# Kernel optimization log

Measured on AMD Instinct MI355X. Metric: run time of the kernel, lower is better.

## Reference

```python
import jax, jax.numpy as jnp
import numpy as np

EMBED_DIM = 1024
NUM_HEADS = 16
HEAD_DIM = EMBED_DIM // NUM_HEADS
B, S = 2, 2048


def setup_inputs() -> dict:
    key = jax.random.key(0)
    ks = jax.random.split(key, 11)
    scale = 1.0 / np.sqrt(EMBED_DIM)
    inp = {
        "q": jax.random.normal(ks[0], (B, S, EMBED_DIM), jnp.float32),
        "k": jax.random.normal(ks[1], (B, S, EMBED_DIM), jnp.float32),
        "v": jax.random.normal(ks[2], (B, S, EMBED_DIM), jnp.float32),
        "Wq": jax.random.normal(ks[3], (EMBED_DIM, EMBED_DIM), jnp.float32) * scale,
        "bq": jnp.zeros((EMBED_DIM,), jnp.float32),
        "Wk": jax.random.normal(ks[4], (EMBED_DIM, EMBED_DIM), jnp.float32) * scale,
        "bk": jnp.zeros((EMBED_DIM,), jnp.float32),
        "Wv": jax.random.normal(ks[5], (EMBED_DIM, EMBED_DIM), jnp.float32) * scale,
        "bv": jnp.zeros((EMBED_DIM,), jnp.float32),
        "Wo": jax.random.normal(ks[6], (EMBED_DIM, EMBED_DIM), jnp.float32) * scale,
        "bo": jnp.zeros((EMBED_DIM,), jnp.float32),
    }
    return inp


def _split_heads(x):
    # [B, S, E] -> [B, H, S, D]
    b, s, _ = x.shape
    return x.reshape(b, s, NUM_HEADS, HEAD_DIM).transpose(0, 2, 1, 3)


def reference(q, k, v, Wq, bq, Wk, bk, Wv, bv, Wo, bo):
    query = _split_heads(q @ Wq + bq)  # [B,H,S,D]
    key_ = _split_heads(k @ Wk + bk)
    value = _split_heads(v @ Wv + bv)
    # scaled dot-product attention (scale by sqrt(head_dim), as in source)
    logits = jnp.einsum("bhqd,bhkd->bhqk", query, key_) / jnp.sqrt(
        jnp.asarray(HEAD_DIM, jnp.float32)
    )
    weights = jax.nn.softmax(logits, axis=-1)
    attn = jnp.einsum("bhqk,bhkd->bhqd", weights, value)  # [B,H,S,D]
    concat = attn.transpose(0, 2, 1, 3).reshape(q.shape[0], -1, EMBED_DIM)
    return concat @ Wo + bo
```

## Files before the change

### kernel.cpp

```cpp
#include <hip/hip_runtime.h>
#include <hip/hip_bf16.h>
#include <math.h>


typedef short bf16x8 __attribute__((ext_vector_type(8)));
typedef short bf16x4 __attribute__((ext_vector_type(4)));
typedef float f32x4 __attribute__((ext_vector_type(4)));
typedef unsigned short u16;
typedef unsigned int u32;

#if defined(__HIP_DEVICE_COMPILE__) && __has_builtin(__builtin_amdgcn_mfma_f32_16x16x16_bf16)
#define MFMA16(a, b, c) __builtin_amdgcn_mfma_f32_16x16x16_bf16(a, b, c, 0, 0, 0)
#else
#define MFMA16(a, b, c) __builtin_amdgcn_mfma_f32_16x16x16bf16_1k(a, b, c, 0, 0, 0)
#endif

#define QSCALE 0.18033688011112042f

__device__ __forceinline__ u16 f2b(float f) {
  union { float f; unsigned u; } v; v.f = f;
  unsigned r = v.u + 0x7FFF + ((v.u >> 16) & 1);
  return (u16)(r >> 16);
}

__device__ __forceinline__ void glds16(const u16* g, u16* l) {
  __builtin_amdgcn_global_load_lds(
      (const __attribute__((address_space(1))) u32*)g,
      (__attribute__((address_space(3))) u32*)l, 16, 0, 0);
}

__global__ void prep(const float* __restrict__ q, const float* __restrict__ k,
                     const float* __restrict__ v, u16* __restrict__ qo,
                     u16* __restrict__ ko, u16* __restrict__ vo,
                     const float* __restrict__ W0, const float* __restrict__ W1,
                     const float* __restrict__ W2, const float* __restrict__ W3,
                     u16* __restrict__ T0, u16* __restrict__ T1,
                     u16* __restrict__ T2, u16* __restrict__ T3) {
  const int z = blockIdx.y;
  if (z < 3) {
    const float* in = z == 0 ? q : (z == 1 ? k : v);
    u16* out = z == 0 ? qo : (z == 1 ? ko : vo);
    int i = (blockIdx.x * 256 + threadIdx.x) * 8;
    float4 a = *(const float4*)(in + i);
    float4 b = *(const float4*)(in + i + 4);
    union { u16 u[8]; uint4 v; } o;
    o.u[0] = f2b(a.x); o.u[1] = f2b(a.y); o.u[2] = f2b(a.z); o.u[3] = f2b(a.w);
    o.u[4] = f2b(b.x); o.u[5] = f2b(b.y); o.u[6] = f2b(b.z); o.u[7] = f2b(b.w);
    *(uint4*)(out + i) = o.v;
    return;
  }
  if (blockIdx.x >= 256) return;
  const int zz = z - 3;
  const float* W = zz == 0 ? W0 : (zz == 1 ? W1 : (zz == 2 ? W2 : W3));
  u16* WT = zz == 0 ? T0 : (zz == 1 ? T1 : (zz == 2 ? T2 : T3));
  __shared__ float tile[64][65];
  int k0 = (blockIdx.x >> 4) * 64, n0 = (blockIdx.x & 15) * 64;
  int c = threadIdx.x & 63, r0 = threadIdx.x >> 6;
  #pragma unroll
  for (int i = 0; i < 64; i += 4)
    tile[r0 + i][c] = W[(k0 + r0 + i) * 1024 + n0 + c];
  __syncthreads();
  #pragma unroll
  for (int i = 0; i < 64; i += 4)
    WT[(n0 + r0 + i) * 1024 + k0 + c] = f2b(tile[c][r0 + i]);
}

template<int MODE, int BN>
__device__ __forceinline__ void gemm_core(
    const u16* __restrict__ A, const u16* __restrict__ BT,
    const float* __restrict__ bias, void* __restrict__ out,
    int bx, int by, float scale) {
  constexpr int NT = BN / 64 * 2;
  __shared__ u16 As[128 * 64];
  __shared__ u16 Bs[BN * 64];
  const int tid = threadIdx.x;
  const int w = tid >> 6, lane = tid & 63;
  const int wm = w >> 1, wn = w & 1;
  const int q = lane >> 4, l16 = lane & 15;
  const int m0 = by * 128, n0 = bx * BN;
  const int K = 1024;

  f32x4 acc[4][NT] = {};
  for (int k0 = 0; k0 < K; k0 += 64) {
    __syncthreads();
    #pragma unroll
    for (int p = 0; p < 4; ++p) {
      int c = p * 4 + w;
      int ci = c * 64 + lane;
      int r = ci >> 3, b = ci & 7;
      glds16(A + (m0 + r) * K + k0 + ((b ^ (r & 7)) * 8), As + c * 512);
    }
    #pragma unroll
    for (int p = 0; p < BN / 32; ++p) {
      int c = p * 4 + w;
      int ci = c * 64 + lane;
      int r = ci >> 3, b = ci & 7;
      glds16(BT + (n0 + r) * K + k0 + ((b ^ (r & 7)) * 8), Bs + c * 512);
    }
    __builtin_amdgcn_s_waitcnt(0xF70);
    __syncthreads();
    #pragma unroll
    for (int ks = 0; ks < 2; ++ks) {
      bf16x8 af[4], bf[NT];
      #pragma unroll
      for (int mt = 0; mt < 4; ++mt) {
        int row = wm * 64 + mt * 16 + l16;
        af[mt] = *(const bf16x8*)(As + row * 64 + (((ks * 4 + q) ^ (row & 7)) * 8));
      }
      #pragma unroll
      for (int nt = 0; nt < NT; ++nt) {
        int row = wn * (BN / 2) + nt * 16 + l16;
        bf[nt] = *(const bf16x8*)(Bs + row * 64 + (((ks * 4 + q) ^ (row & 7)) * 8));
      }
      #pragma unroll
      for (int mt = 0; mt < 4; ++mt)
        #pragma unroll
        for (int nt = 0; nt < NT; ++nt)
          acc[mt][nt] = __builtin_amdgcn_mfma_f32_16x16x32_bf16(af[mt], bf[nt], acc[mt][nt], 0, 0, 0);
    }
  }
  #pragma unroll
  for (int mt = 0; mt < 4; ++mt)
    #pragma unroll
    for (int nt = 0; nt < NT; ++nt) {
      int col = n0 + wn * (BN / 2) + nt * 16 + l16;
      float bcol = bias[col];
      if (MODE == 2) {
        int rbase = m0 + wm * 64 + mt * 16 + q * 4;
        int b = rbase >> 11, s0 = rbase & 2047;
        int h = col >> 6, d = col & 63;
        union { u16 u[4]; uint2 v; } o;
        #pragma unroll
        for (int reg = 0; reg < 4; ++reg)
          o.u[reg] = f2b(acc[mt][nt][reg] + bcol);
        *(uint2*)((u16*)out + (((b << 4) + h) * 64 + d) * 2048 + s0) = o.v;
      } else {
        #pragma unroll
        for (int reg = 0; reg < 4; ++reg) {
          int row = m0 + wm * 64 + mt * 16 + q * 4 + reg;
          float val = (acc[mt][nt][reg] + bcol) * scale;
          if (MODE == 0) {
            int b = row >> 11, s = row & 2047, h = col >> 6, d = col & 63;
            ((u16*)out)[(((b << 4) + h) * 2048 + s) * 64 + d] = f2b(val);
          } else {
            ((float*)out)[row * 1024 + col] = val;
          }
        }
      }
    }
}

__global__ __launch_bounds__(256) void gemm_qkv(
    const u16* qb, const u16* kb, const u16* vb,
    const u16* WqT, const u16* WkT, const u16* WvT,
    const float* bq, const float* bk, const float* bv,
    u16* Qh, u16* Kh, u16* VhT) {
  int z = blockIdx.z;
  if (z == 0)      gemm_core<0, 128>(qb, WqT, bq, Qh,  blockIdx.x, blockIdx.y, QSCALE);
  else if (z == 1) gemm_core<0, 128>(kb, WkT, bk, Kh,  blockIdx.x, blockIdx.y, 1.0f);
  else             gemm_core<2, 128>(vb, WvT, bv, VhT, blockIdx.x, blockIdx.y, 1.0f);
}

__global__ __launch_bounds__(256) void gemm_out(
    const u16* A, const u16* BT, const float* bias, float* out) {
  gemm_core<1, 64>(A, BT, bias, out, blockIdx.x, blockIdx.y, 1.0f);
}

__global__ __launch_bounds__(256) void flash_attn(
    const u16* __restrict__ Qh, const u16* __restrict__ Kh,
    const u16* __restrict__ VTh, u16* __restrict__ Oo) {
  __shared__ u16 Ks[2][4096];
  __shared__ u16 Vt[2][4096];

  const int tid = threadIdx.x, w = tid >> 6, lane = tid & 63;
  const int q = lane >> 4, l16 = lane & 15;
  const int bh = blockIdx.x & 31, qt = blockIdx.x >> 5;
  const u16* Qp = Qh + (bh * 2048 + qt * 128) * 64;
  const u16* Kp = Kh + bh * 2048 * 64;
  const u16* Vp = VTh + bh * 64 * 2048;

  bf16x8 aq[2][2];
  #pragma unroll
  for (int rb = 0; rb < 2; ++rb)
    #pragma unroll
    for (int ks = 0; ks < 2; ++ks)
      aq[rb][ks] = *(const bf16x8*)(Qp + (w * 32 + rb * 16 + l16) * 64 + ks * 32 + q * 8);

  const int sr = (lane & 7) ^ (lane >> 3);
  auto stage = [&](int kt2, int buf) {
    #pragma unroll
    for (int p = 0; p < 2; ++p) {
      int c = p * 4 + w;
      int r = c * 8 + (lane >> 3);
      glds16(Kp + (kt2 * 64 + r) * 64 + sr * 8, &Ks[buf][c * 512]);
      glds16(Vp + r * 2048 + kt2 * 64 + sr * 8, &Vt[buf][c * 512]);
    }
  };
  stage(0, 0);

  f32x4 oacc[4][2] = {};
  float lacc[2] = {0.f, 0.f};

  for (int kt = 0; kt < 32; ++kt) {
    const int buf = kt & 1;
    __builtin_amdgcn_s_waitcnt(0xF70);
    __syncthreads();
    if (kt + 1 < 32) stage(kt + 1, buf ^ 1);

    const u16* KsT = Ks[buf];
    const u16* VtT = Vt[buf];

    f32x4 st[2][4] = {};
    #pragma unroll
    for (int ks = 0; ks < 2; ++ks) {
      bf16x8 bk[4];
      #pragma unroll
      for (int nt = 0; nt < 4; ++nt) {
        int row = nt * 16 + l16;
        bk[nt] = *(const bf16x8*)(KsT + row * 64 + (((ks * 4 + q) ^ (l16 & 7)) * 8));
      }
      #pragma unroll
      for (int rb = 0; rb < 2; ++rb)
        #pragma unroll
        for (int nt = 0; nt < 4; ++nt)
          st[rb][nt] = __builtin_amdgcn_mfma_f32_16x16x32_bf16(bk[nt], aq[rb][ks], st[rb][nt], 0, 0, 0);
    }

    #pragma unroll
    for (int rb = 0; rb < 2; ++rb)
      #pragma unroll
      for (int nt = 0; nt < 4; ++nt)
        #pragma unroll
        for (int reg = 0; reg < 4; ++reg) {
          float p = __builtin_amdgcn_exp2f(st[rb][nt][reg]);
          lacc[rb] += p;
          st[rb][nt][reg] = p;
        }

    #pragma unroll
    for (int kb = 0; kb < 4; ++kb) {
      bf16x4 pf[2];
      #pragma unroll
      for (int rb = 0; rb < 2; ++rb) {
        union { u32 u[2]; bf16x4 v; } pk;
        pk.u[0] = __builtin_amdgcn_perm(__float_as_uint(st[rb][kb][1]),
                                        __float_as_uint(st[rb][kb][0]), 0x07060302u);
        pk.u[1] = __builtin_amdgcn_perm(__float_as_uint(st[rb][kb][3]),
                                        __float_as_uint(st[rb][kb][2]), 0x07060302u);
        pf[rb] = pk.v;
      }
      #pragma unroll
      for (int ntd = 0; ntd < 4; ++ntd) {
        int row = ntd * 16 + l16;
        int c = kb * 2 + (q >> 1);
        bf16x4 vf = *(const bf16x4*)(VtT + row * 64 + ((c ^ (l16 & 7)) * 8) + (q & 1) * 4);
        #pragma unroll
        for (int rb = 0; rb < 2; ++rb)
          oacc[ntd][rb] = MFMA16(vf, pf[rb], oacc[ntd][rb]);
      }
    }
  }

  float rl[2];
  #pragma unroll
  for (int rb = 0; rb < 2; ++rb) {
    float s = lacc[rb];
    s += __shfl_xor(s, 16);
    s += __shfl_xor(s, 32);
    rl[rb] = 0.998046875f / s;
  }

  const int b = bh >> 4, h = bh & 15;
  #pragma unroll
  for (int rb = 0; rb < 2; ++rb) {
    int row = b * 2048 + qt * 128 + w * 32 + rb * 16 + l16;
    #pragma unroll
    for (int ntd = 0; ntd < 4; ++ntd) {
      union { u16 u[4]; uint2 v; } o;
      #pragma unroll
      for (int reg = 0; reg < 4; ++reg)
        o.u[reg] = f2b(oacc[ntd][rb][reg] * rl[rb]);
      *(uint2*)(Oo + row * 1024 + h * 64 + ntd * 16 + q * 4) = o.v;
    }
  }
}

extern "C" void kernel_launch(void* const* d_in, const int* in_sizes, int n_in,
                              void* d_out, int out_size, void* d_ws, size_t ws_size,
                              hipStream_t stream) {
  const float* q  = (const float*)d_in[0];
  const float* k  = (const float*)d_in[1];
  const float* v  = (const float*)d_in[2];
  const float* Wq = (const float*)d_in[3];
  const float* bq = (const float*)d_in[4];
  const float* Wk = (const float*)d_in[5];
  const float* bk = (const float*)d_in[6];
  const float* Wv = (const float*)d_in[7];
  const float* bv = (const float*)d_in[8];
  const float* Wo = (const float*)d_in[9];
  const float* bo = (const float*)d_in[10];

  char* ws = (char*)d_ws;
  const size_t MB = 1024 * 1024;
  u16* qb  = (u16*)(ws);
  u16* kb  = (u16*)(ws + 8 * MB);
  u16* vb  = (u16*)(ws + 16 * MB);
  u16* WqT = (u16*)(ws + 24 * MB);
  u16* WkT = (u16*)(ws + 26 * MB);
  u16* WvT = (u16*)(ws + 28 * MB);
  u16* WoT = (u16*)(ws + 30 * MB);
  u16* Qh  = (u16*)(ws + 32 * MB);
  u16* Kh  = (u16*)(ws + 40 * MB);
  u16* VhT = (u16*)(ws + 48 * MB);
  u16* Ao  = (u16*)(ws + 56 * MB);

  prep<<<dim3(2048, 7), 256, 0, stream>>>(q, k, v, qb, kb, vb,
                                          Wq, Wk, Wv, Wo, WqT, WkT, WvT, WoT);
  gemm_qkv<<<dim3(8, 32, 3), 256, 0, stream>>>(qb, kb, vb, WqT, WkT, WvT,
                                               bq, bk, bv, Qh, Kh, VhT);
  flash_attn<<<512, 256, 0, stream>>>(Qh, Kh, VhT, Ao);
  gemm_out<<<dim3(16, 32), 256, 0, stream>>>(Ao, WoT, bo, (float*)d_out);
}
```

Before: 234.1 us.

## Split attention key range across two blocks and add a combine kernel

Flash attention now launches twice as many blocks. Each block processes half of the key/value sequence and writes unnormalized bf16 partial outputs plus row sums into reused workspace buffers. A new reduce kernel adds the two partials and normalizes them into the attention output. This raises parallelism and occupancy on the many-CU GPU, at the cost of an extra launch, extra global memory traffic for the partials, and bf16 rounding of the partials before they are summed.

Result: slower. 241.1 us (+3.0%).

```diff
diff --git a/kernel.cpp b/kernel.cpp
--- a/kernel.cpp
+++ b/kernel.cpp
@@ -21,6 +21,9 @@
   union { float f; unsigned u; } v; v.f = f;
   unsigned r = v.u + 0x7FFF + ((v.u >> 16) & 1);
   return (u16)(r >> 16);
+}
+__device__ __forceinline__ float b2f(u16 u) {
+  return __uint_as_float(((u32)u) << 16);
 }
 
 __device__ __forceinline__ void glds16(const u16* g, u16* l) {
@@ -168,16 +171,19 @@
 
 __global__ __launch_bounds__(256) void flash_attn(
     const u16* __restrict__ Qh, const u16* __restrict__ Kh,
-    const u16* __restrict__ VTh, u16* __restrict__ Oo) {
+    const u16* __restrict__ VTh, u16* __restrict__ Po0,
+    u16* __restrict__ Po1, float* __restrict__ lP) {
   __shared__ u16 Ks[2][4096];
   __shared__ u16 Vt[2][4096];
 
   const int tid = threadIdx.x, w = tid >> 6, lane = tid & 63;
   const int q = lane >> 4, l16 = lane & 15;
-  const int bh = blockIdx.x & 31, qt = blockIdx.x >> 5;
+  const int bh = blockIdx.x & 31, qt = (blockIdx.x >> 5) & 15;
+  const int half = blockIdx.x >> 9;
   const u16* Qp = Qh + (bh * 2048 + qt * 128) * 64;
-  const u16* Kp = Kh + bh * 2048 * 64;
-  const u16* Vp = VTh + bh * 64 * 2048;
+  const u16* Kp = Kh + bh * 2048 * 64 + half * 1024 * 64;
+  const u16* Vp = VTh + bh * 64 * 2048 + half * 1024;
+  u16* Po = half ? Po1 : Po0;
 
   bf16x8 aq[2][2];
   #pragma unroll
@@ -201,11 +207,11 @@
   f32x4 oacc[4][2] = {};
   float lacc[2] = {0.f, 0.f};
 
-  for (int kt = 0; kt < 32; ++kt) {
+  for (int kt = 0; kt < 16; ++kt) {
     const int buf = kt & 1;
     __builtin_amdgcn_s_waitcnt(0xF70);
     __syncthreads();
-    if (kt + 1 < 32) stage(kt + 1, buf ^ 1);
+    if (kt + 1 < 16) stage(kt + 1, buf ^ 1);
 
     const u16* KsT = Ks[buf];
     const u16* VtT = Vt[buf];
@@ -261,28 +267,40 @@
     }
   }
 
-  float rl[2];
+  const int b = bh >> 4, h = bh & 15;
   #pragma unroll
   for (int rb = 0; rb < 2; ++rb) {
     float s = lacc[rb];
     s += __shfl_xor(s, 16);
     s += __shfl_xor(s, 32);
-    rl[rb] = 0.998046875f / s;
-  }
-
-  const int b = bh >> 4, h = bh & 15;
-  #pragma unroll
-  for (int rb = 0; rb < 2; ++rb) {
-    int row = b * 2048 + qt * 128 + w * 32 + rb * 16 + l16;
+    int rloc = qt * 128 + w * 32 + rb * 16 + l16;
+    if (q == 0) lP[half * 65536 + bh * 2048 + rloc] = s;
+    int row = b * 2048 + rloc;
     #pragma unroll
     for (int ntd = 0; ntd < 4; ++ntd) {
       union { u16 u[4]; uint2 v; } o;
       #pragma unroll
       for (int reg = 0; reg < 4; ++reg)
-        o.u[reg] = f2b(oacc[ntd][rb][reg] * rl[rb]);
-      *(uint2*)(Oo + row * 1024 + h * 64 + ntd * 16 + q * 4) = o.v;
+        o.u[reg] = f2b(oacc[ntd][rb][reg]);
+      *(uint2*)(Po + row * 1024 + h * 64 + ntd * 16 + q * 4) = o.v;
     }
   }
+}
+
+__global__ void reduce_o(const u16* __restrict__ Po0, const u16* __restrict__ Po1,
+                         const float* __restrict__ lP, u16* __restrict__ Ao) {
+  int idx = (blockIdx.x * 256 + threadIdx.x) * 8;
+  int e = idx & 1023, sg = idx >> 10;
+  int b = sg >> 11, s = sg & 2047, h = e >> 6;
+  int li = (b * 16 + h) * 2048 + s;
+  float rl = 0.998046875f / (lP[li] + lP[65536 + li]);
+  union { u16 u[8]; uint4 v; } a, c, o;
+  a.v = *(const uint4*)(Po0 + idx);
+  c.v = *(const uint4*)(Po1 + idx);
+  #pragma unroll
+  for (int i = 0; i < 8; ++i)
+    o.u[i] = f2b((b2f(a.u[i]) + b2f(c.u[i])) * rl);
+  *(uint4*)(Ao + idx) = o.v;
 }
 
 extern "C" void kernel_launch(void* const* d_in, const int* in_sizes, int n_in,
@@ -318,6 +336,9 @@
                                           Wq, Wk, Wv, Wo, WqT, WkT, WvT, WoT);
   gemm_qkv<<<dim3(8, 32, 3), 256, 0, stream>>>(qb, kb, vb, WqT, WkT, WvT,
                                                bq, bk, bv, Qh, Kh, VhT);
-  flash_attn<<<512, 256, 0, stream>>>(Qh, Kh, VhT, Ao);
+  flash_attn<<<1024, 256, 0, stream>>>(Qh, Kh, VhT,
+                                       (u16*)qb, (u16*)kb, (float*)vb);
+  reduce_o<<<2048, 256, 0, stream>>>((const u16*)qb, (const u16*)kb,
+                                     (const float*)vb, Ao);
   gemm_out<<<dim3(16, 32), 256, 0, stream>>>(Ao, WoT, bo, (float*)d_out);
 }
```
